# Kernel optimization log

Hardware: AMD Instinct MI355X
Metric: run time of the kernel (lower is better)

Reference implementation:

```python
import jax, jax.numpy as jnp
import numpy as np

EMBED_DIM = 2048
NUM_Q_HEADS = 16
NUM_KV_HEADS = 4
HEAD_DIM = EMBED_DIM // NUM_Q_HEADS  # 128
N_REP = NUM_Q_HEADS // NUM_KV_HEADS  # 4


def setup_inputs() -> dict:
    key = jax.random.key(0)
    ks = jax.random.split(key, 8)
    B, T, C = 2, 2048, EMBED_DIM
    s = 0.02
    return {
        "x": jax.random.normal(ks[0], (B, T, C), dtype=jnp.float32),
        "Wq": jax.random.normal(ks[1], (C, NUM_Q_HEADS * HEAD_DIM), dtype=jnp.float32) * s,
        "bq": jax.random.normal(ks[2], (NUM_Q_HEADS * HEAD_DIM,), dtype=jnp.float32) * s,
        "Wk": jax.random.normal(ks[3], (C, NUM_KV_HEADS * HEAD_DIM), dtype=jnp.float32) * s,
        "bk": jax.random.normal(ks[4], (NUM_KV_HEADS * HEAD_DIM,), dtype=jnp.float32) * s,
        "Wv": jax.random.normal(ks[5], (C, NUM_KV_HEADS * HEAD_DIM), dtype=jnp.float32) * s,
        "bv": jax.random.normal(ks[6], (NUM_KV_HEADS * HEAD_DIM,), dtype=jnp.float32) * s,
        "Wo": jax.random.normal(ks[7], (C, C), dtype=jnp.float32) * s,
    }


def reference(x, Wq, bq, Wk, bk, Wv, bv, Wo):
    B, T, C = x.shape
    # Projections (torch Linear with bias; weights stored as [in, out])
    q = (x @ Wq + bq).reshape(B, T, NUM_KV_HEADS, N_REP, HEAD_DIM)
    k = (x @ Wk + bk).reshape(B, T, NUM_KV_HEADS, HEAD_DIM)
    v = (x @ Wv + bv).reshape(B, T, NUM_KV_HEADS, HEAD_DIM)
    # GQA: group query heads per kv head instead of materializing repeated K/V.
    # q: [B, G, n_rep, Tq, d], k/v: [B, G, Tk, d]
    q = q.transpose(0, 2, 3, 1, 4)  # B, G, n_rep, T, d
    k = k.transpose(0, 2, 1, 3)     # B, G, T, d
    v = v.transpose(0, 2, 1, 3)
    scale = 1.0 / jnp.sqrt(jnp.asarray(HEAD_DIM, dtype=x.dtype))
    scores = jnp.einsum('bgnqd,bgkd->bgnqk', q, k) * scale
    attn = jax.nn.softmax(scores, axis=-1)
    out = jnp.einsum('bgnqk,bgkd->bgnqd', attn, v)  # B, G, n_rep, T, d
    # merge heads back: (G, n_rep) -> Hq, then [B, T, C]
    out = out.transpose(0, 3, 1, 2, 4).reshape(B, T, C)
    return out @ Wo
```

## Files before the change

kernel.cpp:

```cpp
#include <hip/hip_runtime.h>
#include <hip/hip_bf16.h>
#include <cstdint>
#include <cstddef>

typedef __bf16 bf16;
typedef __attribute__((ext_vector_type(8))) __bf16 bf16x8;
typedef __attribute__((ext_vector_type(4))) float f32x4;
typedef __attribute__((ext_vector_type(16))) float f32x16;

#define KPAD 136
#define VPAD 72

__device__ __forceinline__ void async16(const void* g, void* l) {
  __builtin_amdgcn_global_load_lds(
      (const __attribute__((address_space(1))) void*)g,
      (__attribute__((address_space(3))) void*)l,
      16, 0, 0);
}

__global__ void cvt_x(const float* __restrict__ in, bf16* __restrict__ out, int n8) {
  int i = blockIdx.x * 256 + threadIdx.x;
  if (i >= n8) return;
  const float* src = in + (size_t)i * 8;
  float4 f0 = *reinterpret_cast<const float4*>(src);
  float4 f1 = *reinterpret_cast<const float4*>(src + 4);
  bf16x8 v = {(bf16)f0.x, (bf16)f0.y, (bf16)f0.z, (bf16)f0.w,
              (bf16)f1.x, (bf16)f1.y, (bf16)f1.z, (bf16)f1.w};
  *reinterpret_cast<bf16x8*>(out + (size_t)i * 8) = v;
}

template <typename CT, bool HAS_BIAS>
__global__ __launch_bounds__(256, 2)
void gemm_bt(const bf16* __restrict__ A, const bf16* __restrict__ Bt,
             const bf16* __restrict__ bias, CT* __restrict__ C,
             int M, int N, int K) {
  __shared__ bf16 As[128 * 32];
  __shared__ bf16 Bs[128 * 32];
  const int tid = threadIdx.x;
  const int wave = tid >> 6, lane = tid & 63;
  const int quad = lane >> 4, l15 = lane & 15;
  const int row0 = blockIdx.y * 128;
  const int col0 = blockIdx.x * 128;
  const int wm = wave & 1, wn = wave >> 1;

  const f32x4 fz = {0.f, 0.f, 0.f, 0.f};
  f32x4 acc[4][4];
#pragma unroll
  for (int i = 0; i < 4; ++i)
#pragma unroll
    for (int j = 0; j < 4; ++j) acc[i][j] = fz;

  for (int k0 = 0; k0 < K; k0 += 32) {
    __syncthreads();
#pragma unroll
    for (int j = 0; j < 2; ++j) {
      int c = tid + j * 256;
      int r = c >> 2;
      int kk = (c & 3) * 8;
      async16(A + (size_t)(row0 + r) * K + k0 + kk, &As[c * 8]);
      async16(Bt + (size_t)(col0 + r) * K + k0 + kk, &Bs[c * 8]);
    }
    __syncthreads();

    bf16x8 a[4], b[4];
#pragma unroll
    for (int i = 0; i < 4; ++i)
      a[i] = *reinterpret_cast<const bf16x8*>(&As[(wm * 64 + i * 16 + l15) * 32 + quad * 8]);
#pragma unroll
    for (int j = 0; j < 4; ++j)
      b[j] = *reinterpret_cast<const bf16x8*>(&Bs[(wn * 64 + j * 16 + l15) * 32 + quad * 8]);
#pragma unroll
    for (int i = 0; i < 4; ++i)
#pragma unroll
      for (int j = 0; j < 4; ++j)
        acc[i][j] = __builtin_amdgcn_mfma_f32_16x16x32_bf16(a[i], b[j], acc[i][j], 0, 0, 0);
  }

#pragma unroll
  for (int i = 0; i < 4; ++i) {
    int m = row0 + wm * 64 + i * 16 + quad * 4;
#pragma unroll
    for (int j = 0; j < 4; ++j) {
      int n = col0 + wn * 64 + j * 16 + l15;
      float bv = HAS_BIAS ? (float)bias[n] : 0.f;
#pragma unroll
      for (int r = 0; r < 4; ++r)
        C[(size_t)(m + r) * N + n] = (CT)(acc[i][j][r] + bv);
    }
  }
}

__global__ void transpose2d_cvt(const float* __restrict__ in, bf16* __restrict__ out,
                                int R, int C) {
  __shared__ float t[32][33];
  const int tx = threadIdx.x & 31, ty = threadIdx.x >> 5;
  const int c0 = blockIdx.x * 32, r0 = blockIdx.y * 32;
#pragma unroll
  for (int i = 0; i < 4; ++i)
    t[ty + i * 8][tx] = in[(size_t)(r0 + ty + i * 8) * C + c0 + tx];
  __syncthreads();
#pragma unroll
  for (int i = 0; i < 4; ++i)
    out[(size_t)(c0 + ty + i * 8) * R + r0 + tx] = (bf16)t[tx][ty + i * 8];
}

__global__ void transpose_v(const bf16* __restrict__ QKV, bf16* __restrict__ Vt) {
  const int z = blockIdx.z;
  const int b = z >> 2, g = z & 3;
  const bf16* in = QKV + (size_t)b * 2048 * 3072 + 2560 + g * 128;
  bf16* out = Vt + (size_t)z * 128 * 2048;
  __shared__ bf16 t[32][33];
  const int tx = threadIdx.x & 31, ty = threadIdx.x >> 5;
  const int d0 = blockIdx.x * 32;
  const int t0 = blockIdx.y * 32;
#pragma unroll
  for (int i = 0; i < 4; ++i)
    t[ty + i * 8][tx] = in[(size_t)(t0 + ty + i * 8) * 3072 + d0 + tx];
  __syncthreads();
#pragma unroll
  for (int i = 0; i < 4; ++i)
    out[(size_t)(d0 + ty + i * 8) * 2048 + t0 + tx] = t[tx][ty + i * 8];
}

__global__ void concat_bias(const float* __restrict__ bq, const float* __restrict__ bk,
                            const float* __restrict__ bv, bf16* __restrict__ out) {
  int i = blockIdx.x * 256 + threadIdx.x;
  float v;
  if (i < 2048) v = bq[i];
  else if (i < 2560) v = bk[i - 2048];
  else v = bv[i - 2560];
  out[i] = (bf16)v;
}

__global__ __launch_bounds__(256, 2)
void attn_kernel(const bf16* __restrict__ QKV, const bf16* __restrict__ Vt,
                 bf16* __restrict__ Out) {
  const int bid = blockIdx.x;
  const int qt = bid & 15;
  const int bh = bid >> 4;
  const int b = bh >> 4, h = bh & 15, g = h >> 2;
  const int tid = threadIdx.x;
  const int wave = tid >> 6, lane = tid & 63;
  const int l31 = lane & 31, half = lane >> 5;

  __shared__ bf16 smem[27136];
  bf16* Ks  = smem;
  bf16* Vts = smem + 8704;
  bf16* Ss  = smem + 17920;
  bf16* Qstage = smem;

  const bf16* Qbase = QKV + ((size_t)b * 2048 + qt * 128) * 3072 + h * 128;
#pragma unroll
  for (int j = 0; j < 8; ++j) {
    int c = tid + j * 256;
    *reinterpret_cast<bf16x8*>(&Qstage[(c >> 4) * KPAD + (c & 15) * 8]) =
        *reinterpret_cast<const bf16x8*>(Qbase + (size_t)(c >> 4) * 3072 + (c & 15) * 8);
  }
  __syncthreads();
  bf16x8 qf[8];
#pragma unroll
  for (int ks = 0; ks < 8; ++ks)
    qf[ks] = *reinterpret_cast<const bf16x8*>(
        &Qstage[(wave * 32 + l31) * KPAD + ks * 16 + half * 8]);

  const bf16* Kbase = QKV + (size_t)b * 2048 * 3072 + 2048 + g * 128;
  const bf16* Vbase = Vt + (size_t)(b * 4 + g) * 128 * 2048;

  f32x16 po[4];
#pragma unroll
  for (int j = 0; j < 4; ++j)
#pragma unroll
    for (int r = 0; r < 16; ++r) po[j][r] = 0.f;
  float lsum[16];
#pragma unroll
  for (int r = 0; r < 16; ++r) lsum[r] = 0.f;
  const float sc = 0.08838834764831845f;

  for (int t0 = 0; t0 < 2048; t0 += 64) {
    __syncthreads();
#pragma unroll
    for (int j = 0; j < 4; ++j) {
      int c = tid + j * 256;
      *reinterpret_cast<bf16x8*>(&Ks[(c >> 4) * KPAD + (c & 15) * 8]) =
          *reinterpret_cast<const bf16x8*>(Kbase + (size_t)(t0 + (c >> 4)) * 3072 + (c & 15) * 8);
      *reinterpret_cast<bf16x8*>(&Vts[(c >> 3) * VPAD + (c & 7) * 8]) =
          *reinterpret_cast<const bf16x8*>(Vbase + (size_t)(c >> 3) * 2048 + t0 + (c & 7) * 8);
    }
    __syncthreads();

    f32x16 s[2];
#pragma unroll
    for (int nt = 0; nt < 2; ++nt)
#pragma unroll
      for (int r = 0; r < 16; ++r) s[nt][r] = 0.f;
#pragma unroll
    for (int ks = 0; ks < 8; ++ks) {
#pragma unroll
      for (int nt = 0; nt < 2; ++nt) {
        bf16x8 kf = *reinterpret_cast<const bf16x8*>(
            &Ks[(nt * 32 + l31) * KPAD + ks * 16 + half * 8]);
        s[nt] = __builtin_amdgcn_mfma_f32_32x32x16_bf16(qf[ks], kf, s[nt], 0, 0, 0);
      }
    }

    bf16* SsW = Ss + wave * (32 * VPAD);
#pragma unroll
    for (int nt = 0; nt < 2; ++nt) {
#pragma unroll
      for (int r = 0; r < 16; ++r) {
        float p = __expf(s[nt][r] * sc);
        lsum[r] += p;
        int row = (r & 3) + 8 * (r >> 2) + 4 * half;
        SsW[row * VPAD + nt * 32 + l31] = (bf16)p;
      }
    }

#pragma unroll
    for (int ks2 = 0; ks2 < 4; ++ks2) {
      bf16x8 pf = *reinterpret_cast<const bf16x8*>(
          &SsW[l31 * VPAD + ks2 * 16 + half * 8]);
#pragma unroll
      for (int nt = 0; nt < 4; ++nt) {
        bf16x8 vf = *reinterpret_cast<const bf16x8*>(
            &Vts[(nt * 32 + l31) * VPAD + ks2 * 16 + half * 8]);
        po[nt] = __builtin_amdgcn_mfma_f32_32x32x16_bf16(pf, vf, po[nt], 0, 0, 0);
      }
    }
  }

  const size_t qrow0 = (size_t)b * 2048 + (size_t)qt * 128 + wave * 32;
#pragma unroll
  for (int r = 0; r < 16; ++r) {
    float l = lsum[r];
#pragma unroll
    for (int off = 1; off < 32; off <<= 1) l += __shfl_xor(l, off, 64);
    float inv = 1.0f / l;
    int row = (r & 3) + 8 * (r >> 2) + 4 * half;
#pragma unroll
    for (int nt = 0; nt < 4; ++nt)
      Out[(qrow0 + row) * 2048 + h * 128 + nt * 32 + l31] = (bf16)(po[nt][r] * inv);
  }
}

extern "C" void kernel_launch(void* const* d_in, const int* in_sizes, int n_in,
                              void* d_out, int out_size, void* d_ws, size_t ws_size,
                              hipStream_t stream) {
  const float* x  = (const float*)d_in[0];
  const float* Wq = (const float*)d_in[1];
  const float* bq = (const float*)d_in[2];
  const float* Wk = (const float*)d_in[3];
  const float* bk = (const float*)d_in[4];
  const float* Wv = (const float*)d_in[5];
  const float* bv = (const float*)d_in[6];
  const float* Wo = (const float*)d_in[7];
  float* out = (float*)d_out;
  bf16* ws = (bf16*)d_ws;

  bf16* wqkvT = ws;
  bf16* biasq = ws + 6291456;
  bf16* woT   = ws + 6294528;
  bf16* qkv   = ws + 10488832;
  bf16* vt    = ws + 23071744;
  bf16* aout  = ws + 25168896;
  bf16* xb    = ws + 33557504;

  cvt_x<<<4096, 256, 0, stream>>>(x, xb, 1048576);
  transpose2d_cvt<<<dim3(64, 64), 256, 0, stream>>>(Wq, wqkvT, 2048, 2048);
  transpose2d_cvt<<<dim3(16, 64), 256, 0, stream>>>(Wk, wqkvT + 2048 * 2048, 2048, 512);
  transpose2d_cvt<<<dim3(16, 64), 256, 0, stream>>>(Wv, wqkvT + 2560 * 2048, 2048, 512);
  transpose2d_cvt<<<dim3(64, 64), 256, 0, stream>>>(Wo, woT, 2048, 2048);
  concat_bias<<<12, 256, 0, stream>>>(bq, bk, bv, biasq);

  gemm_bt<bf16, true><<<dim3(24, 32), 256, 0, stream>>>(xb, wqkvT, biasq, qkv, 4096, 3072, 2048);

  transpose_v<<<dim3(4, 64, 8), 256, 0, stream>>>(qkv, vt);

  attn_kernel<<<512, 256, 0, stream>>>(qkv, vt, aout);

  gemm_bt<float, false><<<dim3(16, 32), 256, 0, stream>>>(aout, woT, nullptr, out, 4096, 2048, 2048);
}
```

Before: 322.4 us.

## Prefetch next K/V tile into registers and raise wave priority around MFMA loops

The attention loop now loads the next K and V tiles from global memory into registers right after the LDS barrier, so those loads overlap the current tile's QK^T, softmax and PV compute. Previously the global loads were issued and waited on inside the barrier-bounded stage. It also wraps both MFMA loops in s_setprio(1)/s_setprio(0) to favour matrix-issuing waves. The register prefetch adds about 32 VGPRs per thread, which can reduce occupancy.

Result: slower. 334.7 us (+3.8%).

```diff
diff --git a/kernel.cpp b/kernel.cpp
--- a/kernel.cpp
+++ b/kernel.cpp
@@ -166,6 +166,16 @@
   const bf16* Kbase = QKV + (size_t)b * 2048 * 3072 + 2048 + g * 128;
   const bf16* Vbase = Vt + (size_t)(b * 4 + g) * 128 * 2048;
 
+  bf16x8 kreg[4], vreg[4];
+#pragma unroll
+  for (int j = 0; j < 4; ++j) {
+    int c = tid + j * 256;
+    kreg[j] = *reinterpret_cast<const bf16x8*>(
+        Kbase + (size_t)(c >> 4) * 3072 + (c & 15) * 8);
+    vreg[j] = *reinterpret_cast<const bf16x8*>(
+        Vbase + (size_t)(c >> 3) * 2048 + (c & 7) * 8);
+  }
+
   f32x16 po[4];
 #pragma unroll
   for (int j = 0; j < 4; ++j)
@@ -181,18 +191,29 @@
 #pragma unroll
     for (int j = 0; j < 4; ++j) {
       int c = tid + j * 256;
-      *reinterpret_cast<bf16x8*>(&Ks[(c >> 4) * KPAD + (c & 15) * 8]) =
-          *reinterpret_cast<const bf16x8*>(Kbase + (size_t)(t0 + (c >> 4)) * 3072 + (c & 15) * 8);
-      *reinterpret_cast<bf16x8*>(&Vts[(c >> 3) * VPAD + (c & 7) * 8]) =
-          *reinterpret_cast<const bf16x8*>(Vbase + (size_t)(c >> 3) * 2048 + t0 + (c & 7) * 8);
+      *reinterpret_cast<bf16x8*>(&Ks[(c >> 4) * KPAD + (c & 15) * 8]) = kreg[j];
+      *reinterpret_cast<bf16x8*>(&Vts[(c >> 3) * VPAD + (c & 7) * 8]) = vreg[j];
     }
     __syncthreads();
 
+    if (t0 + 64 < 2048) {
+      const int t1 = t0 + 64;
+#pragma unroll
+      for (int j = 0; j < 4; ++j) {
+        int c = tid + j * 256;
+        kreg[j] = *reinterpret_cast<const bf16x8*>(
+            Kbase + (size_t)(t1 + (c >> 4)) * 3072 + (c & 15) * 8);
+        vreg[j] = *reinterpret_cast<const bf16x8*>(
+            Vbase + (size_t)(c >> 3) * 2048 + t1 + (c & 7) * 8);
+      }
+    }
+
     f32x16 s[2];
 #pragma unroll
     for (int nt = 0; nt < 2; ++nt)
 #pragma unroll
       for (int r = 0; r < 16; ++r) s[nt][r] = 0.f;
+    __builtin_amdgcn_s_setprio(1);
 #pragma unroll
     for (int ks = 0; ks < 8; ++ks) {
 #pragma unroll
@@ -202,6 +223,7 @@
         s[nt] = __builtin_amdgcn_mfma_f32_32x32x16_bf16(qf[ks], kf, s[nt], 0, 0, 0);
       }
     }
+    __builtin_amdgcn_s_setprio(0);
 
     bf16* SsW = Ss + wave * (32 * VPAD);
 #pragma unroll
@@ -215,6 +237,7 @@
       }
     }
 
+    __builtin_amdgcn_s_setprio(1);
 #pragma unroll
     for (int ks2 = 0; ks2 < 4; ++ks2) {
       bf16x8 pf = *reinterpret_cast<const bf16x8*>(
@@ -226,6 +249,7 @@
         po[nt] = __builtin_amdgcn_mfma_f32_32x32x16_bf16(pf, vf, po[nt], 0, 0, 0);
       }
     }
+    __builtin_amdgcn_s_setprio(0);
   }
 
   const size_t qrow0 = (size_t)b * 2048 + (size_t)qt * 128 + wave * 32;
```

## Keep softmax probabilities in registers via transposed QK MFMA and permlane swap

Applied to the files above, without the earlier changes.

The QK^T MFMA operands are swapped so each lane holds scores for a single query row. The probabilities are then packed to bf16 in registers and rearranged with v_permlane32_swap to form the A operand of the PV MFMA, instead of going through an LDS staging buffer. This removes the per-tile LDS writes and reads of P, reduces shared memory, and turns the row-sum reduction into a single cross-half shuffle. It relies on inline asm for gfx950-specific instructions and on the exact MFMA register layout being correct.

Result: faster. 309.8 us (-3.9%).

```diff
diff --git a/kernel.cpp b/kernel.cpp
--- a/kernel.cpp
+++ b/kernel.cpp
@@ -143,10 +143,9 @@
   const int wave = tid >> 6, lane = tid & 63;
   const int l31 = lane & 31, half = lane >> 5;
 
-  __shared__ bf16 smem[27136];
+  __shared__ bf16 smem[17920];
   bf16* Ks  = smem;
   bf16* Vts = smem + 8704;
-  bf16* Ss  = smem + 17920;
   bf16* Qstage = smem;
 
   const bf16* Qbase = QKV + ((size_t)b * 2048 + qt * 128) * 3072 + h * 128;
@@ -171,9 +170,7 @@
   for (int j = 0; j < 4; ++j)
 #pragma unroll
     for (int r = 0; r < 16; ++r) po[j][r] = 0.f;
-  float lsum[16];
-#pragma unroll
-  for (int r = 0; r < 16; ++r) lsum[r] = 0.f;
+  float lsum = 0.f;
   const float sc = 0.08838834764831845f;
 
   for (int t0 = 0; t0 < 2048; t0 += 64) {
@@ -199,46 +196,53 @@
       for (int nt = 0; nt < 2; ++nt) {
         bf16x8 kf = *reinterpret_cast<const bf16x8*>(
             &Ks[(nt * 32 + l31) * KPAD + ks * 16 + half * 8]);
-        s[nt] = __builtin_amdgcn_mfma_f32_32x32x16_bf16(qf[ks], kf, s[nt], 0, 0, 0);
+        s[nt] = __builtin_amdgcn_mfma_f32_32x32x16_bf16(kf, qf[ks], s[nt], 0, 0, 0);
       }
     }
 
-    bf16* SsW = Ss + wave * (32 * VPAD);
-#pragma unroll
-    for (int nt = 0; nt < 2; ++nt) {
+#pragma unroll
+    for (int nt = 0; nt < 2; ++nt)
 #pragma unroll
       for (int r = 0; r < 16; ++r) {
         float p = __expf(s[nt][r] * sc);
-        lsum[r] += p;
-        int row = (r & 3) + 8 * (r >> 2) + 4 * half;
-        SsW[row * VPAD + nt * 32 + l31] = (bf16)p;
+        lsum += p;
+        s[nt][r] = p;
       }
-    }
 
 #pragma unroll
     for (int ks2 = 0; ks2 < 4; ++ks2) {
-      bf16x8 pf = *reinterpret_cast<const bf16x8*>(
-          &SsW[l31 * VPAD + ks2 * 16 + half * 8]);
-#pragma unroll
-      for (int nt = 0; nt < 4; ++nt) {
+      const int nt = ks2 >> 1;
+      const int a = (ks2 & 1) * 8;
+      uint32_t x0, x1, x2, x3;
+      asm("v_cvt_pk_bf16_f32 %0, %1, %2" : "=v"(x0) : "v"(s[nt][a + 0]), "v"(s[nt][a + 1]));
+      asm("v_cvt_pk_bf16_f32 %0, %1, %2" : "=v"(x1) : "v"(s[nt][a + 2]), "v"(s[nt][a + 3]));
+      asm("v_cvt_pk_bf16_f32 %0, %1, %2" : "=v"(x2) : "v"(s[nt][a + 4]), "v"(s[nt][a + 5]));
+      asm("v_cvt_pk_bf16_f32 %0, %1, %2" : "=v"(x3) : "v"(s[nt][a + 6]), "v"(s[nt][a + 7]));
+      asm("v_permlane32_swap_b32 %0, %1" : "+v"(x0), "+v"(x2));
+      asm("v_permlane32_swap_b32 %0, %1" : "+v"(x1), "+v"(x3));
+      union { uint32_t u[4]; bf16x8 v; } pu;
+      pu.u[0] = x0; pu.u[1] = x1; pu.u[2] = x2; pu.u[3] = x3;
+      const bf16x8 pf = pu.v;
+#pragma unroll
+      for (int nd = 0; nd < 4; ++nd) {
         bf16x8 vf = *reinterpret_cast<const bf16x8*>(
-            &Vts[(nt * 32 + l31) * VPAD + ks2 * 16 + half * 8]);
-        po[nt] = __builtin_amdgcn_mfma_f32_32x32x16_bf16(pf, vf, po[nt], 0, 0, 0);
+            &Vts[(nd * 32 + l31) * VPAD + ks2 * 16 + half * 8]);
+        po[nd] = __builtin_amdgcn_mfma_f32_32x32x16_bf16(pf, vf, po[nd], 0, 0, 0);
       }
     }
   }
 
+  float l = lsum + __shfl_xor(lsum, 32, 64);
+  float inv = 1.0f / l;
+
   const size_t qrow0 = (size_t)b * 2048 + (size_t)qt * 128 + wave * 32;
 #pragma unroll
   for (int r = 0; r < 16; ++r) {
-    float l = lsum[r];
-#pragma unroll
-    for (int off = 1; off < 32; off <<= 1) l += __shfl_xor(l, off, 64);
-    float inv = 1.0f / l;
     int row = (r & 3) + 8 * (r >> 2) + 4 * half;
+    float invr = __shfl(inv, row, 64);
 #pragma unroll
     for (int nt = 0; nt < 4; ++nt)
-      Out[(qrow0 + row) * 2048 + h * 128 + nt * 32 + l31] = (bf16)(po[nt][r] * inv);
+      Out[(qrow0 + row) * 2048 + h * 128 + nt * 32 + l31] = (bf16)(po[nt][r] * invr);
   }
 }
 
```
